# Kernel tuning notes

Measured on AMD Instinct MI355X. Metric: run time of the kernel, lower is better.

Reference implementation:

```python
import jax, jax.numpy as jnp
import numpy as np

MAX_RES = 5.0  # max_residue_magnitude
DG = 16       # deform_groups
KH = KW = 3
K = KH * KW
PAD = 1
STRIDE = 1
DIL = 1


def conv3x3(x, w, b):
    y = jax.lax.conv_general_dilated(
        x, w, window_strides=(1, 1), padding='SAME',
        dimension_numbers=('NCHW', 'OIHW', 'NCHW'))
    return y + b[None, :, None, None]


def lrelu(x):
    return jnp.where(x >= 0, x, 0.1 * x)


def deform_conv2d(x, offset, mask, weight, bias):
    # x: [B,C,H,W]; offset: [B,2*DG*K,Ho,Wo]; mask: [B,DG*K,Ho,Wo]
    B, C, H, W = x.shape
    Cout = weight.shape[0]
    Ho = (H + 2 * PAD - DIL * (KH - 1) - 1) // STRIDE + 1
    Wo = (W + 2 * PAD - DIL * (KW - 1) - 1) // STRIDE + 1
    Cg = C // DG

    # torchvision layout: offset channel = g*(2*K) + 2*k + {0:y, 1:x}
    off = offset.reshape(B, DG, K, 2, Ho, Wo)
    oy, ox = off[:, :, :, 0], off[:, :, :, 1]           # [B,DG,K,Ho,Wo]
    msk = mask.reshape(B, DG, K, Ho, Wo)

    ki = DIL * (jnp.arange(K) // KW)                    # [K] kernel row offsets
    kj = DIL * (jnp.arange(K) % KW)
    base_y = STRIDE * jnp.arange(Ho) - PAD              # [Ho]
    base_x = STRIDE * jnp.arange(Wo) - PAD              # [Wo]
    py = base_y[None, None, None, :, None] + ki[None, None, :, None, None] + oy
    px = base_x[None, None, None, None, :] + kj[None, None, :, None, None] + ox

    xg = x.reshape(B, DG, Cg, H * W)

    y0 = jnp.floor(py)
    x0 = jnp.floor(px)
    wy1 = py - y0
    wx1 = px - x0

    def corner(iy, ix, w_c):
        valid = ((iy >= 0) & (iy <= H - 1) & (ix >= 0) & (ix <= W - 1)).astype(x.dtype)
        iyc = jnp.clip(iy, 0, H - 1).astype(jnp.int32)
        ixc = jnp.clip(ix, 0, W - 1).astype(jnp.int32)
        idx = (iyc * W + ixc).reshape(B, DG, 1, K * Ho * Wo)
        g = jnp.take_along_axis(
            xg, jnp.broadcast_to(idx, (B, DG, Cg, K * Ho * Wo)), axis=3)
        g = g.reshape(B, DG, Cg, K, Ho, Wo)
        return g * (w_c * valid)[:, :, None]

    val = (corner(y0, x0, (1 - wy1) * (1 - wx1))
           + corner(y0, x0 + 1, (1 - wy1) * wx1)
           + corner(y0 + 1, x0, wy1 * (1 - wx1))
           + corner(y0 + 1, x0 + 1, wy1 * wx1))

    val = val * msk[:, :, None]                          # modulation
    val = val.reshape(B, C, K, Ho, Wo)                   # columns
    out = jnp.einsum('bckhw,ock->bohw', val, weight.reshape(Cout, C, K))
    return out + bias[None, :, None, None]


def setup_inputs() -> dict:
    key = jax.random.key(0)
    ks = jax.random.split(key, 12)
    B, H, W = 1, 192, 192
    inp = {
        'x':    jax.random.normal(ks[0], (B, 128, H, W), jnp.float32),
        'cond': jax.random.normal(ks[1], (B, 192, H, W), jnp.float32),
        'weight': jax.random.normal(ks[2], (64, 128, 3, 3), jnp.float32) * 0.03,
        'bias':   jax.random.normal(ks[3], (64,), jnp.float32) * 0.01,
        'w1': jax.random.normal(ks[4], (64, 192, 3, 3), jnp.float32) * 0.03,
        'b1': jax.random.normal(ks[5], (64,), jnp.float32) * 0.01,
        'w2': jax.random.normal(ks[6], (64, 64, 3, 3), jnp.float32) * 0.05,
        'b2': jax.random.normal(ks[7], (64,), jnp.float32) * 0.01,
        'w3': jax.random.normal(ks[8], (64, 64, 3, 3), jnp.float32) * 0.05,
        'b3': jax.random.normal(ks[9], (64,), jnp.float32) * 0.01,
        'w4': jax.random.normal(ks[10], (432, 64, 3, 3), jnp.float32) * 0.05,
        'b4': jax.random.normal(ks[11], (432,), jnp.float32) * 0.01,
    }
    return inp


def reference(x, cond, weight, bias, w1, b1, w2, b2, w3, b3, w4, b4):
    h = lrelu(conv3x3(cond, w1, b1))
    h = lrelu(conv3x3(h, w2, b2))
    h = lrelu(conv3x3(h, w3, b3))
    out = conv3x3(h, w4, b4)                       # [B, 27*DG, H, W]
    offset, mask = out[:, :18 * DG], out[:, 18 * DG:]
    offset = MAX_RES * jnp.tanh(offset)
    mask = jax.nn.sigmoid(mask)
    return deform_conv2d(x, offset, mask, weight, bias)
```

## Files before the change

### kernel.cpp

```cpp
#include <hip/hip_runtime.h>
#include <hip/hip_bf16.h>
#include <math.h>

#define IMG_H 192
#define IMG_W 192
#define NPIX (IMG_H * IMG_W)
#define PADW 194
#define PPIX (PADW * PADW)
#define PH 208
#define PW 208

typedef _Float16 h8 __attribute__((ext_vector_type(8)));
typedef _Float16 h4 __attribute__((ext_vector_type(4)));
typedef float f32x4 __attribute__((ext_vector_type(4)));

__device__ __forceinline__ float act_tanh5(float x) {
    const float t = __expf(2.f * x);
    return 5.f * (t - 1.f) / (t + 1.f);
}
__device__ __forceinline__ float act_sig(float x) {
    return 1.f / (1.f + __expf(-x));
}

typedef __attribute__((address_space(1))) const unsigned int GU32;
typedef __attribute__((address_space(3))) unsigned int LU32;
__device__ __forceinline__ void cp16(const void* g, void* l) {
    __builtin_amdgcn_global_load_lds((GU32*)g, (LU32*)l, 16, 0, 0);
}

template<int CIN, int COP, int COUT>
__device__ __forceinline__ void pack_body(
    int bx, const float* __restrict__ src, _Float16* __restrict__ dst)
{
    const int chunk = bx / 9, k = bx % 9;
    for (int i = threadIdx.x; i < COP * 32; i += 256) {
        const int co = i >> 5, cil = i & 31;
        float v = 0.f;
        if (co < COUT)
            v = src[((size_t)(co * CIN + chunk * 32 + cil)) * 9 + k];
        dst[(size_t)bx * COP * 32 + i] = (_Float16)v;
    }
}

__global__ __launch_bounds__(256) void prep_all_k(
    const float* __restrict__ cond, const float* __restrict__ w1,
    const float* __restrict__ w2, const float* __restrict__ w3,
    const float* __restrict__ w4, const float* __restrict__ x,
    const float* __restrict__ weight,
    _Float16* __restrict__ act_cond, _Float16* __restrict__ wp1,
    _Float16* __restrict__ wp2, _Float16* __restrict__ wp3,
    _Float16* __restrict__ wp4, _Float16* __restrict__ xg,
    _Float16* __restrict__ wdg, _Float16* __restrict__ pb_all)
{
    int b = blockIdx.x;
    const int t = threadIdx.x;

    if (b < 1164) {
        const int y = b % 194;
        const int c = b / 194;
        if (t >= PADW) return;
        const bool inb = (y >= 1 && y <= IMG_H && t >= 1 && t <= IMG_W);
        h8 v[4];
#pragma unroll
        for (int j = 0; j < 32; j++)
            ((_Float16*)v)[j] = inb
                ? (_Float16)cond[(size_t)(c * 32 + j) * NPIX + (y - 1) * IMG_W + (t - 1)]
                : (_Float16)0.f;
        h8* d = (h8*)&act_cond[((size_t)c * PPIX + (size_t)y * PADW + t) * 32];
        d[0] = v[0]; d[1] = v[1]; d[2] = v[2]; d[3] = v[3];
        return;
    }
    b -= 1164;

    if (b < 3072) {
        const int y  = b % 192;
        const int dg = b / 192;
        if (t < 192) {
            h8 v;
#pragma unroll
            for (int chl = 0; chl < 8; chl++)
                v[chl] = (_Float16)x[(size_t)(dg * 8 + chl) * NPIX + y * IMG_W + t];
            *(h8*)&xg[(((size_t)dg * PH + y + 6) * PW + t + 6) * 8] = v;
        }
        return;
    }
    b -= 3072;

    if (b < 108) {
        if      (b < 54) pack_body<192, 64, 64>(b, w1, wp1);
        else if (b < 72) pack_body<64, 64, 64>(b - 54, w2, wp2);
        else if (b < 90) pack_body<64, 64, 64>(b - 72, w3, wp3);
        else             pack_body<64, 448, 432>(b - 90, w4, wp4);
        return;
    }
    b -= 108;

    if (b < 384) {
        const int i = b * 256 + t;
        if (i < 16 * 64 * 96) {
            const int ks = i % 96;
            const int rest = i / 96;
            const int co = rest % 64;
            const int dg = rest / 64;
            const int k = ks >> 3, chl = ks & 7;
            float v = 0.f;
            if (ks < 72)
                v = weight[((size_t)co * 128 + dg * 8 + chl) * 9 + k];
            wdg[i] = (_Float16)v;
        }
        return;
    }
    b -= 384;

    if (b < 400) {
        const int idx = b * 256 + t;
        if (idx < 16 * 6400) {
            const int dg = idx / 6400;
            int r = idx % 6400;
            int row, col;
            if (r < 1248)      { row = r / 208;              col = r % 208; }
            else if (r < 3328) { r -= 1248; row = 198 + r / 208; col = r % 208; }
            else if (r < 4480) { r -= 3328; row = 6 + r / 6;     col = r % 6; }
            else               { r -= 4480; row = 6 + r / 10;    col = 198 + r % 10; }
            h8 z = {0, 0, 0, 0, 0, 0, 0, 0};
            *(h8*)&xg[(((size_t)dg * PH + row) * PW + col) * 8] = z;
        }
        return;
    }
    b -= 400;

    {
        const int idx = b * 256 + t;
        if (idx < 6 * 772 * 4) {
            const int px_id = idx >> 2, part = idx & 3;
            const int plane = px_id / 772;
            int r = px_id % 772;
            int y, xx;
            if (r < 194)      { y = 0;            xx = r; }
            else if (r < 388) { y = 193;          xx = r - 194; }
            else if (r < 580) { y = 1 + (r - 388); xx = 0; }
            else              { y = 1 + (r - 580); xx = 193; }
            h8 z = {0, 0, 0, 0, 0, 0, 0, 0};
            *(h8*)&pb_all[((size_t)plane * PPIX + (size_t)y * PADW + xx) * 32 + part * 8] = z;
        }
        return;
    }
}

template<int CHUNKS, int ACT, int COP, int T8>
__global__ __launch_bounds__(256) void conv_lds_k(
    const _Float16* __restrict__ in,
    const _Float16* __restrict__ wpk,
    const float* __restrict__ bias,
    _Float16* __restrict__ out)
{
    constexpr int HALO = T8 ? 10 : 18;
    constexpr int NF   = T8 ? 1 : 4;
    constexpr int TDIM = T8 ? 24 : 12;
    constexpr int TSZ  = T8 ? 8 : 16;
    constexpr int INU  = HALO * HALO * 4;
    constexpr int ROWU = HALO * 4;

    __shared__ _Float16 in_lds[HALO * HALO * 32];
    __shared__ _Float16 w_lds[9 * 64 * 32];

    const int t    = threadIdx.x;
    const int lane = t & 63;
    const int wv   = __builtin_amdgcn_readfirstlane(t >> 6);
    const int col  = lane & 15;
    const int quad = lane >> 4;
    const int bx   = blockIdx.x;
    const int tx0  = (bx % TDIM) * TSZ;
    const int ty0  = (bx / TDIM) * TSZ;
    const int cobase = blockIdx.y * 64;

    f32x4 acc[4][NF];
#pragma unroll
    for (int m = 0; m < 4; m++)
#pragma unroll
        for (int s = 0; s < NF; s++) {
            f32x4 z = {0.f, 0.f, 0.f, 0.f};
            acc[m][s] = z;
        }

    for (int c = 0; c < CHUNKS; c++) {
        __syncthreads();
        {
            const char* gbase = (const char*)in + (size_t)c * PPIX * 64;
            char* lbase = (char*)in_lds + (size_t)wv * 64 * 16;
#pragma unroll
            for (int i = 0; i < (INU + 255) / 256; i++) {
                const int j = t + i * 256;
                if (j < INU) {
                    const int row = j / ROWU;
                    const int u   = j - row * ROWU;
                    cp16(gbase + ((size_t)(ty0 + row) * PADW + tx0) * 64 + u * 16,
                         lbase + (size_t)i * 256 * 16);
                }
            }
        }
        {
            const char* gw = (const char*)wpk
                + ((size_t)(c * 9) * COP + cobase) * 64 + t * 16;
            char* lw = (char*)w_lds + (size_t)wv * 64 * 16;
#pragma unroll
            for (int k = 0; k < 9; k++)
                cp16(gw + (size_t)k * COP * 64, lw + k * 4096);
        }
        __syncthreads();

#pragma unroll
        for (int k = 0; k < 9; k++) {
            const int ky = k / 3, kx = k % 3;
            h8 af[4];
#pragma unroll
            for (int m = 0; m < 4; m++)
                af[m] = *(const h8*)&w_lds[(k * 64 + m * 16 + col) * 32 + quad * 8];
            h8 bf[NF];
            if (T8) {
                bf[0] = *(const h8*)&in_lds[
                    ((2 * wv + (col >> 3) + ky) * HALO + (col & 7) + kx) * 32 + quad * 8];
            } else {
#pragma unroll
                for (int s = 0; s < NF; s++)
                    bf[s] = *(const h8*)&in_lds[
                        ((4 * wv + s + ky) * HALO + col + kx) * 32 + quad * 8];
            }
#pragma unroll
            for (int m = 0; m < 4; m++)
#pragma unroll
                for (int s = 0; s < NF; s++)
                    acc[m][s] = __builtin_amdgcn_mfma_f32_16x16x32_f16(
                        af[m], bf[s], acc[m][s], 0, 0, 0);
        }
    }

#pragma unroll
    for (int m = 0; m < 4; m++) {
#pragma unroll
        for (int s = 0; s < NF; s++) {
            int gy, gx;
            if (T8) { gy = ty0 + 2 * wv + (col >> 3); gx = tx0 + (col & 7); }
            else    { gy = ty0 + 4 * wv + s;          gx = tx0 + col; }
            const int ca = cobase + m * 16 + quad * 4;
            if (ACT == 1) {
                h4 st;
#pragma unroll
                for (int r = 0; r < 4; r++) {
                    float v = acc[m][s][r] + bias[ca + r];
                    st[r] = (_Float16)((v >= 0.f) ? v : 0.1f * v);
                }
                *(h4*)&out[((size_t)(ca >> 5) * PPIX + (size_t)(gy + 1) * PADW + (gx + 1)) * 32
                           + (ca & 31)] = st;
            } else {
#pragma unroll
                for (int r = 0; r < 4; r++) {
                    const int co = ca + r;
                    if (co < 432) {
                        const int pix = gy * IMG_W + gx;
                        out[((size_t)(pix >> 5) * 432 + co) * 32 + (pix & 31)] =
                            (_Float16)(acc[m][s][r] + bias[co]);
                    }
                }
            }
        }
    }
}

__global__ __launch_bounds__(256) void deform_mfma_k(
    const _Float16* __restrict__ xg,
    const _Float16* __restrict__ od,
    const _Float16* __restrict__ wdg,
    const float* __restrict__ bias,
    float* __restrict__ out)
{
    __shared__ __align__(16) _Float16 val4[4][32][104];

    const int t    = threadIdx.x;
    const int lane = t & 63;
    const int wv   = __builtin_amdgcn_readfirstlane(t >> 6);
    const int col  = lane & 15;
    const int quad = lane >> 4;
    const int bxr  = blockIdx.x;
    const int bx   = (bxr & 7) * 144 + (bxr >> 3);
    const int gy   = bx / 6;
    const int gx0  = (bx % 6) * 32;

    const _Float16* odseg = od + (size_t)bx * 432 * 32;

    for (int i = t; i < 4 * 32 * 4; i += 256) {
        const int dgl = i >> 7;
        const int r   = i & 127;
        const int px  = r >> 2;
        const int j   = r & 3;
        h8 z = {0, 0, 0, 0, 0, 0, 0, 0};
        *(h8*)&val4[dgl][px][72 + 8 * j] = z;
    }

    f32x4 acc[2];
    {
        f32x4 z = {0.f, 0.f, 0.f, 0.f};
        acc[0] = z; acc[1] = z;
    }

    for (int dq = 0; dq < 4; dq++) {
        __syncthreads();

        for (int idx = t; idx < 1152; idx += 256) {
            const int pxl  = idx & 31;
            const int rest = idx >> 5;
            const int k    = rest % 9;
            const int dgl  = rest / 9;
            const int dg   = dq * 4 + dgl;
            const int rr   = dgl * 9 + k;
            const float oy = act_tanh5((float)odseg[(dq * 72 + 2 * rr) * 32 + pxl]);
            const float ox = act_tanh5((float)odseg[(dq * 72 + 2 * rr + 1) * 32 + pxl]);
            const float m  = act_sig((float)odseg[(288 + dq * 36 + rr) * 32 + pxl]);
            const float py  = (float)(gy - 1 + k / 3) + oy;
            const float pxx = (float)(gx0 + pxl - 1 + k % 3) + ox;
            const float y0 = floorf(py), x0 = floorf(pxx);
            const float fy = py - y0, fx = pxx - x0;
            const int iy = (int)y0 + 6, ix = (int)x0 + 6;
            const _Float16* p = xg + (((size_t)dg * PH + iy) * PW + ix) * 8;
            const h8 c00 = *(const h8*)p;
            const h8 c01 = *(const h8*)(p + 8);
            const h8 c10 = *(const h8*)(p + PW * 8);
            const h8 c11 = *(const h8*)(p + PW * 8 + 8);
            const float ey = 1.f - fy, ex = 1.f - fx;
            const _Float16 s00 = (_Float16)(ey * ex * m);
            const _Float16 s01 = (_Float16)(ey * fx * m);
            const _Float16 s10 = (_Float16)(fy * ex * m);
            const _Float16 s11 = (_Float16)(fy * fx * m);
            const h8 v = c00 * s00 + c01 * s01 + c10 * s10 + c11 * s11;
            *(h8*)&val4[dgl][pxl][k * 8] = v;
        }
        __syncthreads();

#pragma unroll
        for (int dgl = 0; dgl < 4; dgl++) {
            const int dg = dq * 4 + dgl;
            const _Float16* wbase = wdg + ((size_t)dg * 64 + wv * 16 + col) * 96;
#pragma unroll
            for (int ks = 0; ks < 3; ks++) {
                const h8 a  = *(const h8*)(wbase + ks * 32 + quad * 8);
                const h8 b0 = *(const h8*)&val4[dgl][col][ks * 32 + quad * 8];
                const h8 b1 = *(const h8*)&val4[dgl][16 + col][ks * 32 + quad * 8];
                acc[0] = __builtin_amdgcn_mfma_f32_16x16x32_f16(a, b0, acc[0], 0, 0, 0);
                acc[1] = __builtin_amdgcn_mfma_f32_16x16x32_f16(a, b1, acc[1], 0, 0, 0);
            }
        }
    }

    const int co = wv * 16 + quad * 4;
#pragma unroll
    for (int n = 0; n < 2; n++) {
        const int gx = gx0 + n * 16 + col;
#pragma unroll
        for (int r = 0; r < 4; r++)
            out[(size_t)(co + r) * NPIX + gy * IMG_W + gx] = acc[n][r] + bias[co + r];
    }
}

extern "C" void kernel_launch(void* const* d_in, const int* in_sizes, int n_in,
                              void* d_out, int out_size, void* d_ws, size_t ws_size,
                              hipStream_t stream) {
    (void)in_sizes; (void)n_in; (void)out_size; (void)ws_size;

    const float* x      = (const float*)d_in[0];
    const float* cond   = (const float*)d_in[1];
    const float* weight = (const float*)d_in[2];
    const float* bias   = (const float*)d_in[3];
    const float* w1     = (const float*)d_in[4];
    const float* b1     = (const float*)d_in[5];
    const float* w2     = (const float*)d_in[6];
    const float* b2     = (const float*)d_in[7];
    const float* w3     = (const float*)d_in[8];
    const float* b3     = (const float*)d_in[9];
    const float* w4     = (const float*)d_in[10];
    const float* b4     = (const float*)d_in[11];
    float* out = (float*)d_out;

    char* ws = (char*)d_ws;
    size_t off = 0;
    auto take = [&](size_t bytes) -> char* {
        char* p = ws + off;
        off = (off + bytes + 255) & ~(size_t)255;
        return p;
    };
    _Float16* act_cond = (_Float16*)take((size_t)6 * PPIX * 32 * 2);
    _Float16* pb_all   = (_Float16*)take((size_t)3 * 2 * PPIX * 32 * 2);
    _Float16* pb1 = pb_all;
    _Float16* pb2 = pb1 + (size_t)2 * PPIX * 32;
    _Float16* pb3 = pb2 + (size_t)2 * PPIX * 32;
    _Float16* od  = (_Float16*)take((size_t)432 * NPIX * 2);
    _Float16* wp1 = (_Float16*)take((size_t)54 * 64 * 32 * 2);
    _Float16* wp2 = (_Float16*)take((size_t)18 * 64 * 32 * 2);
    _Float16* wp3 = (_Float16*)take((size_t)18 * 64 * 32 * 2);
    _Float16* wp4 = (_Float16*)take((size_t)18 * 448 * 32 * 2);
    _Float16* xg  = (_Float16*)take((size_t)16 * PH * PW * 8 * 2);
    _Float16* wdg = (_Float16*)take((size_t)16 * 64 * 96 * 2);

    hipLaunchKernelGGL(prep_all_k, dim3(5201), dim3(256), 0, stream,
                       cond, w1, w2, w3, w4, x, weight,
                       act_cond, wp1, wp2, wp3, wp4, xg, wdg, pb_all);

    hipLaunchKernelGGL((conv_lds_k<6, 1, 64, 1>),  dim3(576, 1), dim3(256), 0, stream, act_cond, wp1, b1, pb1);
    hipLaunchKernelGGL((conv_lds_k<2, 1, 64, 1>),  dim3(576, 1), dim3(256), 0, stream, pb1, wp2, b2, pb2);
    hipLaunchKernelGGL((conv_lds_k<2, 1, 64, 1>),  dim3(576, 1), dim3(256), 0, stream, pb2, wp3, b3, pb3);
    hipLaunchKernelGGL((conv_lds_k<2, 2, 448, 0>), dim3(144, 7), dim3(256), 0, stream, pb3, wp4, b4, od);
    hipLaunchKernelGGL(deform_mfma_k, dim3(1152), dim3(256), 0, stream, xg, od, wdg, bias, out);
}
```

Measured before the change: 240.6 us.

## Stage deform input window in LDS via async copies and fuse offset activations into conv

Moves the tanh/sigmoid activation of offsets and masks into the epilogue of the final conv kernel, so the deform kernel reads already-activated values. The deform kernel now copies a 13x45 input window per deform group into shared memory with async 16-byte copies, prefetching the next group-quad while MFMAs run. Bilinear corner gathers then come from LDS instead of scattered global loads. The cost is extra LDS use (about 37 KB), which may lower occupancy, and the window bounds assume offsets stay within ±5.

```diff
diff --git a/kernel.cpp b/kernel.cpp
--- a/kernel.cpp
+++ b/kernel.cpp
@@ -258,8 +258,10 @@
                     const int co = ca + r;
                     if (co < 432) {
                         const int pix = gy * IMG_W + gx;
+                        float v = acc[m][s][r] + bias[co];
+                        v = (ca < 288) ? act_tanh5(v) : act_sig(v);
                         out[((size_t)(pix >> 5) * 432 + co) * 32 + (pix & 31)] =
-                            (_Float16)(acc[m][s][r] + bias[co]);
+                            (_Float16)v;
                     }
                 }
             }
@@ -275,6 +277,7 @@
     float* __restrict__ out)
 {
     __shared__ __align__(16) _Float16 val4[4][32][104];
+    __shared__ __align__(16) _Float16 wnd[4][13][45 * 8];
 
     const int t    = threadIdx.x;
     const int lane = t & 63;
@@ -297,11 +300,31 @@
         *(h8*)&val4[dgl][px][72 + 8 * j] = z;
     }
 
+    auto stage = [&](int dq) {
+        const int base_dg = dq * 4;
+        char* lbase = (char*)wnd + (size_t)wv * 64 * 16;
+#pragma unroll
+        for (int i = 0; i < 10; i++) {
+            const int j = t + i * 256;
+            if (i < 9 || j < 2340) {
+                const int dgl = j / 585;
+                const int rem = j - dgl * 585;
+                const int wr  = rem / 45;
+                const int u   = rem - wr * 45;
+                cp16((const char*)xg
+                         + (((size_t)(base_dg + dgl) * PH + gy + wr) * PW + gx0 + u) * 16,
+                     lbase + (size_t)i * 256 * 16);
+            }
+        }
+    };
+
     f32x4 acc[2];
     {
         f32x4 z = {0.f, 0.f, 0.f, 0.f};
         acc[0] = z; acc[1] = z;
     }
+
+    stage(0);
 
     for (int dq = 0; dq < 4; dq++) {
         __syncthreads();
@@ -311,21 +334,23 @@
             const int rest = idx >> 5;
             const int k    = rest % 9;
             const int dgl  = rest / 9;
-            const int dg   = dq * 4 + dgl;
             const int rr   = dgl * 9 + k;
-            const float oy = act_tanh5((float)odseg[(dq * 72 + 2 * rr) * 32 + pxl]);
-            const float ox = act_tanh5((float)odseg[(dq * 72 + 2 * rr + 1) * 32 + pxl]);
-            const float m  = act_sig((float)odseg[(288 + dq * 36 + rr) * 32 + pxl]);
+            const float oy = (float)odseg[(dq * 72 + 2 * rr) * 32 + pxl];
+            const float ox = (float)odseg[(dq * 72 + 2 * rr + 1) * 32 + pxl];
+            const float m  = (float)odseg[(288 + dq * 36 + rr) * 32 + pxl];
             const float py  = (float)(gy - 1 + k / 3) + oy;
             const float pxx = (float)(gx0 + pxl - 1 + k % 3) + ox;
             const float y0 = floorf(py), x0 = floorf(pxx);
             const float fy = py - y0, fx = pxx - x0;
-            const int iy = (int)y0 + 6, ix = (int)x0 + 6;
-            const _Float16* p = xg + (((size_t)dg * PH + iy) * PW + ix) * 8;
+            const int ly = (int)y0 - (gy - 6);
+            const int lc = (int)x0 - (gx0 - 6);
+            const int ly1 = (ly < 12) ? ly + 1 : 12;
+            const _Float16* p  = &wnd[dgl][ly][lc * 8];
+            const _Float16* p1 = &wnd[dgl][ly1][lc * 8];
             const h8 c00 = *(const h8*)p;
             const h8 c01 = *(const h8*)(p + 8);
-            const h8 c10 = *(const h8*)(p + PW * 8);
-            const h8 c11 = *(const h8*)(p + PW * 8 + 8);
+            const h8 c10 = *(const h8*)p1;
+            const h8 c11 = *(const h8*)(p1 + 8);
             const float ey = 1.f - fy, ex = 1.f - fx;
             const _Float16 s00 = (_Float16)(ey * ex * m);
             const _Float16 s01 = (_Float16)(ey * fx * m);
@@ -335,6 +360,8 @@
             *(h8*)&val4[dgl][pxl][k * 8] = v;
         }
         __syncthreads();
+
+        if (dq < 3) stage(dq + 1);
 
 #pragma unroll
         for (int dgl = 0; dgl < 4; dgl++) {
```

Measured after the change: 253.1 us. 5.2% more time.
